# Performance work log

Hardware: AMD Instinct MI355X
Metric: run time of the kernel (lower is better)

## Reference

```python
import jax, jax.numpy as jnp
import numpy as np

IMAGE_SIZE = 288.0
LAMBDA_NOOBJ = 0.5
LAMBDA_COOR = 5.0
_ANCHOR_DIMS = np.array([[0.24, 0.24], [0.12, 0.12], [0.08, 0.08], [0.28, 0.28], [0.15, 0.15]], np.float32)
ANCHORS = jnp.concatenate([jnp.full((5, 2), 0.5, jnp.float32), jnp.asarray(_ANCHOR_DIMS)], axis=1)  # [cx,cy,w,h]


def _corners(box):
    # matches torch _format_bbox column order used in _get_iou: (x1, x2, y1, y2)
    cx, cy, w, h = box[..., 0], box[..., 1], box[..., 2], box[..., 3]
    return cx - w / 2, cx + w / 2, cy - h / 2, cy + h / 2


def _iou(b1, b2):
    x1a, x2a, y1a, y2a = _corners(b1)
    x1b, x2b, y1b, y2b = _corners(b2)
    iw = jnp.minimum(x2a, x2b) - jnp.maximum(x1a, x1b) + 1.0
    ih = jnp.minimum(y2a, y2b) - jnp.maximum(y1a, y1b) + 1.0
    inter = iw * ih
    a1 = (x2a - x1a + 1.0) * (y2a - y1a + 1.0)
    a2 = (x2b - x1b + 1.0) * (y2b - y1b + 1.0)
    return inter / (a1 + a2 - inter + 1e-16)


def setup_inputs() -> dict:
    key = jax.random.key(0)
    k1, k2, k3, k4 = jax.random.split(key, 4)
    B, G, A, T = 32, 36, 5, 8
    return {
        "bbox_prediction": jax.random.normal(k1, (B, G, G, A, 5), jnp.float32),
        "landmarks_prediction": jax.random.normal(k2, (B, G, G, A, 68, 2), jnp.float32),
        "bbox_target": jax.random.uniform(k3, (B, T, 4), jnp.float32),
        "landmarks_target": jax.random.uniform(k4, (B, T, 68, 2), jnp.float32),
    }


def _forward(bbox_prediction, landmarks_prediction, bbox_target, landmarks_target):
    B, G, _, A, _ = bbox_prediction.shape
    T = bbox_target.shape[1]
    N = B * G * G * A

    valid = bbox_target.sum(-1) != 0  # (B,T)
    gx = bbox_target[..., 0] * G
    gy = bbox_target[..., 1] * G
    gi = jnp.floor(gx).astype(jnp.int32)  # int(gt_x)
    gj = jnp.floor(gy).astype(jnp.int32)
    fx = gx - gi
    fy = gy - gj
    gt_anchor_box = jnp.stack([fx, fy, bbox_target[..., 2], bbox_target[..., 3]], -1)  # (B,T,4)

    # vectorized anchor assignment (replaces per-target python loop)
    anchor_iou = _iou(gt_anchor_box[:, :, None, :], ANCHORS[None, None, :, :])  # (B,T,A)
    best_a = jnp.argmax(anchor_iou, -1).astype(jnp.int32)
    log_box = jnp.log1p(gt_anchor_box)  # (B,T,4) -- torch stores log1p form

    lin = ((jnp.arange(B)[:, None] * G + gj) * G + gi) * A + best_a  # (B,T) flat (b,j,i,a)
    lin = jnp.where(valid, lin, N)  # invalid targets -> dump slot N

    obj = jnp.zeros(N + 1, jnp.float32).at[lin.ravel()].set(1.0)[:N].reshape(B, G, G, A)
    noobj = 1.0 - obj

    t_ids = jnp.broadcast_to(jnp.arange(T, dtype=jnp.int32), (B, T))
    seg_last = jax.ops.segment_max(t_ids.ravel(), lin.ravel(), num_segments=N + 1)
    winner = (seg_last[lin] == t_ids) & valid
    lin_w = jnp.where(winner, lin, N).ravel()

    gt_boxes = jnp.zeros((N + 1, 4), jnp.float32).at[lin_w].set(log_box.reshape(-1, 4))[:N].reshape(B, G, G, A, 4)
    gt_lm = jnp.zeros((N + 1, 136), jnp.float32).at[lin_w].set(landmarks_target.reshape(B * T, 136))[:N].reshape(B, G, G, A, 136)

    nobj = jnp.maximum(obj.sum(), 1.0)

    # NME over object cells (masked-mean expressed as weighted sum -> static shapes)
    diff = landmarks_prediction.reshape(B, G, G, A, 136) - gt_lm
    dist = jnp.sqrt(jnp.sum(diff * diff, -1))  # (B,G,G,A)
    wh = gt_boxes[..., 2] * gt_boxes[..., 3]  # note: log1p(w)*log1p(h), as in torch
    norm = jnp.sqrt(jnp.where(obj > 0, wh, 1.0)) * IMAGE_SIZE * 68.0 * nobj
    nme = jnp.sum(obj * dist / norm)

    # localization: SmoothL1 (beta=1), mean over masked elements
    d = bbox_prediction[..., :4] - gt_boxes
    ad = jnp.abs(d)
    sl1 = jnp.where(ad < 1.0, 0.5 * d * d, ad - 0.5)
    loc_loss = LAMBDA_COOR * jnp.sum(obj[..., None] * sl1) / (nobj * 4.0)

    # confidence: MSE on noobj (target 0) + MSE on obj (target 1)
    conf_pred = bbox_prediction[..., 4]
    n_noobj = jnp.maximum(noobj.sum(), 1.0)
    conf_loss = LAMBDA_NOOBJ * jnp.sum(noobj * conf_pred ** 2) / n_noobj + jnp.sum(obj * (conf_pred - 1.0) ** 2) / nobj

    # best predicted bbox per target (IoU of log1p gt box vs raw cell predictions, as in torch)
    cell_pred = bbox_prediction[jnp.arange(B)[:, None], gj, gi]  # (B,T,A,5)
    pred_iou = _iou(log_box[:, :, None, :], cell_pred[..., :4])  # (B,T,A)
    best_p = jnp.argmax(pred_iou, -1)
    best = jnp.take_along_axis(cell_pred, best_p[..., None, None], axis=2)[:, :, 0]  # (B,T,5)
    x1, x2, y1, y2 = _corners(best[..., :4])
    best_pred = jnp.where(valid[..., None], jnp.stack([x1, x2, y1, y2, best[..., 4]], -1), 0.0)

    return nme, loc_loss, conf_loss, best_pred


def reference(bbox_prediction, landmarks_prediction, bbox_target, landmarks_target):
    return _forward(bbox_prediction, landmarks_prediction, bbox_target, landmarks_target)
```

## Files before the change

### kernel.cpp

```cpp
#include <hip/hip_runtime.h>
#include <math.h>

#define Gc 36
#define Ac 5
#define Bc 32
#define Tc 8
#define NCELLS (Bc*Gc*Gc*Ac)
#define NFLOATS (NCELLS*5)
#define NF4 (NFLOATS/4)
#define NT 256
#define CONF_BLOCKS 128


__device__ __forceinline__ void target_meta(const float* __restrict__ bbox_tgt,
                                            int tid, bool& valid, int& gi, int& gj,
                                            float& fx, float& fy, float& w, float& h,
                                            int& best_a) {
    const int b = tid >> 3, t = tid & 7;
    const float* tg = bbox_tgt + (size_t)(b * Tc + t) * 4;
    float x = tg[0], y = tg[1];
    w = tg[2]; h = tg[3];
    valid = ((x + y + w + h) != 0.0f);
    float gx = x * (float)Gc, gy = y * (float)Gc;
    gi = (int)floorf(gx); gj = (int)floorf(gy);
    gi = min(max(gi, 0), Gc - 1); gj = min(max(gj, 0), Gc - 1);
    fx = gx - floorf(gx); fy = gy - floorf(gy);

    float x1a = fx - w * 0.5f, x2a = fx + w * 0.5f;
    float y1a = fy - h * 0.5f, y2a = fy + h * 0.5f;
    float a1 = (x2a - x1a + 1.0f) * (y2a - y1a + 1.0f);
    const float adim[Ac] = {0.24f, 0.12f, 0.08f, 0.28f, 0.15f};
    best_a = 0;
    float best_iou = -1e30f;
    for (int a = 0; a < Ac; ++a) {
        float x1b = 0.5f - adim[a] * 0.5f, x2b = 0.5f + adim[a] * 0.5f;
        float iw = fminf(x2a, x2b) - fmaxf(x1a, x1b) + 1.0f;
        float ih = fminf(y2a, x2b) - fmaxf(y1a, x1b) + 1.0f;
        float inter = iw * ih;
        float a2 = (x2b - x1b + 1.0f) * (x2b - x1b + 1.0f);
        float iou = inter / (a1 + a2 - inter + 1e-16f);
        if (iou > best_iou) { best_iou = iou; best_a = a; }
    }
}

__global__ __launch_bounds__(NT) void k1_conf_meta(
        const float* __restrict__ bbox_pred,
        const float* __restrict__ bbox_tgt,
        float* __restrict__ ws_f, int* __restrict__ ws_i) {
    if (blockIdx.x < CONF_BLOCKS) {
        __shared__ float red[NT];
        const float4* p4 = (const float4*)bbox_pred;
        float acc = 0.0f;
        for (int j = blockIdx.x * NT + threadIdx.x; j < NF4;
             j += CONF_BLOCKS * NT) {
            float4 f = p4[j];
            int r = (4 * j) % 5;
            float v = (r == 4) ? f.x : (r == 3) ? f.y : (r == 2) ? f.z
                    : (r == 1) ? f.w : 0.0f;
            acc += v * v;
        }
        red[threadIdx.x] = acc;
        __syncthreads();
        for (int s = NT / 2; s > 0; s >>= 1) {
            if (threadIdx.x < s) red[threadIdx.x] += red[threadIdx.x + s];
            __syncthreads();
        }
        if (threadIdx.x == 0) ws_f[blockIdx.x] = red[0];
    } else {
        __shared__ int s_lin[NT];
        const int tid = threadIdx.x;
        const int b = tid >> 3, t = tid & 7;
        bool valid; int gi, gj, best_a; float fx, fy, w, h;
        target_meta(bbox_tgt, tid, valid, gi, gj, fx, fy, w, h, best_a);
        int lin = valid ? (((b * Gc + gj) * Gc + gi) * Ac + best_a) : NCELLS;
        s_lin[tid] = lin;
        __syncthreads();
        bool winner = valid;
        if (valid) {
            for (int t2 = t + 1; t2 < Tc; ++t2)
                if (s_lin[(b << 3) + t2] == lin) { winner = false; break; }
        }
        ws_i[256 + tid] = lin;
        ws_i[512 + tid] = winner ? 1 : 0;
    }
}

__global__ __launch_bounds__(64) void k2_lmdist(
        const float* __restrict__ lm_pred,
        const float* __restrict__ lm_tgt,
        const int* __restrict__ ws_i,
        float* __restrict__ ws_f) {
    const int tgt = blockIdx.x;
    const int lane = threadIdx.x;
    int winner = ws_i[512 + tgt];
    int lin = ws_i[256 + tgt];
    float acc = 0.0f;
    if (winner && lane < 34) {
        const float4* lp = (const float4*)(lm_pred + (size_t)lin * 136);
        const float4* lt = (const float4*)(lm_tgt + (size_t)tgt * 136);
        float4 a = lp[lane], b = lt[lane];
        float dx = a.x - b.x, dy = a.y - b.y, dz = a.z - b.z, dw = a.w - b.w;
        acc = dx * dx + dy * dy + dz * dz + dw * dw;
    }
    for (int off = 32; off > 0; off >>= 1)
        acc += __shfl_down(acc, off, 64);
    if (lane == 0) ws_f[1024 + tgt] = winner ? sqrtf(acc) : 0.0f;
}

__device__ __forceinline__ float block_sum(float v, float* red, int tid) {
    red[tid] = v;
    __syncthreads();
    for (int s = NT / 2; s > 0; s >>= 1) {
        if (tid < s) red[tid] += red[tid + s];
        __syncthreads();
    }
    float r = red[0];
    __syncthreads();
    return r;
}

__global__ __launch_bounds__(NT) void k3_final(
        const float* __restrict__ bbox_pred,
        const float* __restrict__ bbox_tgt,
        const float* __restrict__ ws_f,
        const int* __restrict__ ws_i,
        float* __restrict__ out) {
    const int tid = threadIdx.x;
    const int b = tid >> 3, t = tid & 7;
    __shared__ float s_red[NT];
    __shared__ int s_cnt[NT];

    bool valid; int gi, gj, best_a; float fx, fy, w, h;
    target_meta(bbox_tgt, tid, valid, gi, gj, fx, fy, w, h, best_a);
    int lin = ws_i[256 + tid];
    int winner = ws_i[512 + tid];
    float dist = ws_f[1024 + tid];

    float l0 = log1pf(fx), l1 = log1pf(fy), l2 = log1pf(w), l3 = log1pf(h);

    float c_nme = 0.0f, c_sl1 = 0.0f, c_cobj = 0.0f, c_csq = 0.0f;
    if (winner) {
        const float* bp = bbox_pred + (size_t)lin * 5;
        float conf = bp[4];
        c_cobj = (conf - 1.0f) * (conf - 1.0f);
        c_csq = conf * conf;
        float lb[4] = {l0, l1, l2, l3};
        for (int k = 0; k < 4; ++k) {
            float d = bp[k] - lb[k];
            float ad = fabsf(d);
            c_sl1 += (ad < 1.0f) ? 0.5f * d * d : (ad - 0.5f);
        }
        c_nme = dist / (sqrtf(l2 * l3) * 288.0f * 68.0f);
    }

    s_cnt[tid] = winner;
    __syncthreads();
    for (int s = NT / 2; s > 0; s >>= 1) {
        if (tid < s) s_cnt[tid] += s_cnt[tid + s];
        __syncthreads();
    }
    int cnt = s_cnt[0];
    __syncthreads();
    float nobj = fmaxf((float)cnt, 1.0f);
    float n_noobj = fmaxf((float)(NCELLS - cnt), 1.0f);

    float sum_nme  = block_sum(c_nme, s_red, tid);
    float sum_sl1  = block_sum(c_sl1, s_red, tid);
    float sum_cobj = block_sum(c_cobj, s_red, tid);
    float sum_csq  = block_sum(c_csq, s_red, tid);
    float s_total  = block_sum(tid < CONF_BLOCKS ? ws_f[tid] : 0.0f, s_red, tid);

    if (tid == 0) {
        out[0] = sum_nme / nobj;
        out[1] = 5.0f * sum_sl1 / (nobj * 4.0f);
        out[2] = 0.5f * (s_total - sum_csq) / n_noobj + sum_cobj / nobj;
    }

    const float* cp = bbox_pred + (size_t)((b * Gc + gj) * Gc + gi) * Ac * 5;
    float x1g = l0 - l2 * 0.5f, x2g = l0 + l2 * 0.5f;
    float y1g = l1 - l3 * 0.5f, y2g = l1 + l3 * 0.5f;
    float ag = (x2g - x1g + 1.0f) * (y2g - y1g + 1.0f);
    int bp_idx = 0;
    float bp_iou = -1e30f;
    for (int a = 0; a < Ac; ++a) {
        float cx = cp[a * 5 + 0], cy = cp[a * 5 + 1];
        float pw = cp[a * 5 + 2], ph = cp[a * 5 + 3];
        float x1p = cx - pw * 0.5f, x2p = cx + pw * 0.5f;
        float y1p = cy - ph * 0.5f, y2p = cy + ph * 0.5f;
        float iw = fminf(x2g, x2p) - fmaxf(x1g, x1p) + 1.0f;
        float ih = fminf(y2g, y2p) - fmaxf(y1g, y1p) + 1.0f;
        float inter = iw * ih;
        float ap = (x2p - x1p + 1.0f) * (y2p - y1p + 1.0f);
        float iou = inter / (ag + ap - inter + 1e-16f);
        if (iou > bp_iou) { bp_iou = iou; bp_idx = a; }
    }
    float bx = cp[bp_idx * 5 + 0], by = cp[bp_idx * 5 + 1];
    float bw = cp[bp_idx * 5 + 2], bh = cp[bp_idx * 5 + 3];
    float bconf = cp[bp_idx * 5 + 4];
    float* op = out + 3 + (size_t)tid * 5;
    if (valid) {
        op[0] = bx - bw * 0.5f; op[1] = bx + bw * 0.5f;
        op[2] = by - bh * 0.5f; op[3] = by + bh * 0.5f; op[4] = bconf;
    } else {
        op[0] = 0.0f; op[1] = 0.0f; op[2] = 0.0f; op[3] = 0.0f; op[4] = 0.0f;
    }
}

extern "C" void kernel_launch(void* const* d_in, const int* in_sizes, int n_in,
                              void* d_out, int out_size, void* d_ws, size_t ws_size,
                              hipStream_t stream) {
    const float* bbox_pred = (const float*)d_in[0];
    const float* lm_pred   = (const float*)d_in[1];
    const float* bbox_tgt  = (const float*)d_in[2];
    const float* lm_tgt    = (const float*)d_in[3];
    float* out = (float*)d_out;
    float* ws_f = (float*)d_ws;
    int* ws_i = (int*)d_ws;

    k1_conf_meta<<<CONF_BLOCKS + 1, NT, 0, stream>>>(bbox_pred, bbox_tgt, ws_f, ws_i);
    k2_lmdist<<<256, 64, 0, stream>>>(lm_pred, lm_tgt, ws_i, ws_f);
    k3_final<<<1, NT, 0, stream>>>(bbox_pred, bbox_tgt, ws_f, ws_i, out);
}
```

Baseline: 159.0 us.

## Fuse three kernels into one with atomic last-block finalization

Replaces the three-kernel pipeline (confidence reduction plus target metadata, landmark distance, final reduction) with a single 256-block kernel. Each block does a slice of the confidence sum-of-squares, computes metadata and the landmark distance for one target, and accumulates into workspace through atomics. The last block to finish writes the scalar losses. This removes two kernel launches and their inter-kernel dependencies, at the cost of a memset, float atomics with nondeterministic summation order, and dropping the gi/gj clamp.

```diff
diff --git a/kernel.cpp b/kernel.cpp
--- a/kernel.cpp
+++ b/kernel.cpp
@@ -6,24 +6,21 @@
 #define Bc 32
 #define Tc 8
 #define NCELLS (Bc*Gc*Gc*Ac)
-#define NFLOATS (NCELLS*5)
-#define NF4 (NFLOATS/4)
+#define NF4 (NCELLS*5/4)
 #define NT 256
-#define CONF_BLOCKS 128
+#define NB 256
 
 
 __device__ __forceinline__ void target_meta(const float* __restrict__ bbox_tgt,
-                                            int tid, bool& valid, int& gi, int& gj,
+                                            int tgt, bool& valid, int& gi, int& gj,
                                             float& fx, float& fy, float& w, float& h,
                                             int& best_a) {
-    const int b = tid >> 3, t = tid & 7;
-    const float* tg = bbox_tgt + (size_t)(b * Tc + t) * 4;
+    const float* tg = bbox_tgt + (size_t)tgt * 4;
     float x = tg[0], y = tg[1];
     w = tg[2]; h = tg[3];
     valid = ((x + y + w + h) != 0.0f);
     float gx = x * (float)Gc, gy = y * (float)Gc;
     gi = (int)floorf(gx); gj = (int)floorf(gy);
-    gi = min(max(gi, 0), Gc - 1); gj = min(max(gj, 0), Gc - 1);
     fx = gx - floorf(gx); fy = gy - floorf(gy);
 
     float x1a = fx - w * 0.5f, x2a = fx + w * 0.5f;
@@ -43,166 +40,136 @@
     }
 }
 
-__global__ __launch_bounds__(NT) void k1_conf_meta(
+__global__ __launch_bounds__(NT) void fused(
         const float* __restrict__ bbox_pred,
+        const float* __restrict__ lm_pred,
         const float* __restrict__ bbox_tgt,
-        float* __restrict__ ws_f, int* __restrict__ ws_i) {
-    if (blockIdx.x < CONF_BLOCKS) {
-        __shared__ float red[NT];
-        const float4* p4 = (const float4*)bbox_pred;
-        float acc = 0.0f;
-        for (int j = blockIdx.x * NT + threadIdx.x; j < NF4;
-             j += CONF_BLOCKS * NT) {
-            float4 f = p4[j];
-            int r = (4 * j) % 5;
-            float v = (r == 4) ? f.x : (r == 3) ? f.y : (r == 2) ? f.z
-                    : (r == 1) ? f.w : 0.0f;
-            acc += v * v;
-        }
-        red[threadIdx.x] = acc;
-        __syncthreads();
-        for (int s = NT / 2; s > 0; s >>= 1) {
-            if (threadIdx.x < s) red[threadIdx.x] += red[threadIdx.x + s];
-            __syncthreads();
-        }
-        if (threadIdx.x == 0) ws_f[blockIdx.x] = red[0];
-    } else {
-        __shared__ int s_lin[NT];
-        const int tid = threadIdx.x;
-        const int b = tid >> 3, t = tid & 7;
-        bool valid; int gi, gj, best_a; float fx, fy, w, h;
-        target_meta(bbox_tgt, tid, valid, gi, gj, fx, fy, w, h, best_a);
-        int lin = valid ? (((b * Gc + gj) * Gc + gi) * Ac + best_a) : NCELLS;
-        s_lin[tid] = lin;
-        __syncthreads();
-        bool winner = valid;
-        if (valid) {
-            for (int t2 = t + 1; t2 < Tc; ++t2)
-                if (s_lin[(b << 3) + t2] == lin) { winner = false; break; }
-        }
-        ws_i[256 + tid] = lin;
-        ws_i[512 + tid] = winner ? 1 : 0;
+        const float* __restrict__ lm_tgt,
+        float* __restrict__ ws_f, int* __restrict__ ws_i,
+        float* __restrict__ out) {
+    const int tid = threadIdx.x;
+    const int bid = blockIdx.x;
+    __shared__ float red[NT];
+    __shared__ int s_lin8[8];
+
+    const float4* p4 = (const float4*)bbox_pred;
+    float acc = 0.0f;
+    for (int j = bid * NT + tid; j < NF4; j += NB * NT) {
+        float4 f = p4[j];
+        int r = (4 * j) % 5;
+        float v = (r == 4) ? f.x : (r == 3) ? f.y : (r == 2) ? f.z
+                : (r == 1) ? f.w : 0.0f;
+        acc += v * v;
     }
-}
-
-__global__ __launch_bounds__(64) void k2_lmdist(
-        const float* __restrict__ lm_pred,
-        const float* __restrict__ lm_tgt,
-        const int* __restrict__ ws_i,
-        float* __restrict__ ws_f) {
-    const int tgt = blockIdx.x;
-    const int lane = threadIdx.x;
-    int winner = ws_i[512 + tgt];
-    int lin = ws_i[256 + tgt];
-    float acc = 0.0f;
-    if (winner && lane < 34) {
-        const float4* lp = (const float4*)(lm_pred + (size_t)lin * 136);
-        const float4* lt = (const float4*)(lm_tgt + (size_t)tgt * 136);
-        float4 a = lp[lane], b = lt[lane];
-        float dx = a.x - b.x, dy = a.y - b.y, dz = a.z - b.z, dw = a.w - b.w;
-        acc = dx * dx + dy * dy + dz * dz + dw * dw;
-    }
-    for (int off = 32; off > 0; off >>= 1)
-        acc += __shfl_down(acc, off, 64);
-    if (lane == 0) ws_f[1024 + tgt] = winner ? sqrtf(acc) : 0.0f;
-}
-
-__device__ __forceinline__ float block_sum(float v, float* red, int tid) {
-    red[tid] = v;
+    red[tid] = acc;
     __syncthreads();
     for (int s = NT / 2; s > 0; s >>= 1) {
         if (tid < s) red[tid] += red[tid + s];
         __syncthreads();
     }
-    float r = red[0];
+
+    const int tgt = bid;
+    const int b = tgt >> 3, t = tgt & 7;
+    if (tid < 8) {
+        bool v; int gi, gj, ba; float fx, fy, w, h;
+        target_meta(bbox_tgt, (b << 3) + tid, v, gi, gj, fx, fy, w, h, ba);
+        s_lin8[tid] = v ? (((b * Gc + gj) * Gc + gi) * Ac + ba) : NCELLS;
+    }
     __syncthreads();
-    return r;
-}
 
-__global__ __launch_bounds__(NT) void k3_final(
-        const float* __restrict__ bbox_pred,
-        const float* __restrict__ bbox_tgt,
-        const float* __restrict__ ws_f,
-        const int* __restrict__ ws_i,
-        float* __restrict__ out) {
-    const int tid = threadIdx.x;
-    const int b = tid >> 3, t = tid & 7;
-    __shared__ float s_red[NT];
-    __shared__ int s_cnt[NT];
+    if (tid < 64) {
+        int lin = s_lin8[t];
+        bool valid = (lin != NCELLS);
+        bool winner = valid;
+        if (valid)
+            for (int t2 = t + 1; t2 < Tc; ++t2)
+                if (s_lin8[t2] == lin) { winner = false; break; }
 
-    bool valid; int gi, gj, best_a; float fx, fy, w, h;
-    target_meta(bbox_tgt, tid, valid, gi, gj, fx, fy, w, h, best_a);
-    int lin = ws_i[256 + tid];
-    int winner = ws_i[512 + tid];
-    float dist = ws_f[1024 + tid];
+        float a2 = 0.0f;
+        if (winner && tid < 34) {
+            const float4* lp = (const float4*)(lm_pred + (size_t)lin * 136);
+            const float4* lt = (const float4*)(lm_tgt + (size_t)tgt * 136);
+            float4 a = lp[tid], c = lt[tid];
+            float dx = a.x - c.x, dy = a.y - c.y, dz = a.z - c.z, dw = a.w - c.w;
+            a2 = dx * dx + dy * dy + dz * dz + dw * dw;
+        }
+        for (int off = 32; off > 0; off >>= 1)
+            a2 += __shfl_down(a2, off, 64);
 
-    float l0 = log1pf(fx), l1 = log1pf(fy), l2 = log1pf(w), l3 = log1pf(h);
+        if (tid == 0) {
+            bool v; int gi, gj, ba; float fx, fy, w, h;
+            target_meta(bbox_tgt, tgt, v, gi, gj, fx, fy, w, h, ba);
+            float l0 = log1pf(fx), l1 = log1pf(fy), l2 = log1pf(w), l3 = log1pf(h);
 
-    float c_nme = 0.0f, c_sl1 = 0.0f, c_cobj = 0.0f, c_csq = 0.0f;
-    if (winner) {
-        const float* bp = bbox_pred + (size_t)lin * 5;
-        float conf = bp[4];
-        c_cobj = (conf - 1.0f) * (conf - 1.0f);
-        c_csq = conf * conf;
-        float lb[4] = {l0, l1, l2, l3};
-        for (int k = 0; k < 4; ++k) {
-            float d = bp[k] - lb[k];
-            float ad = fabsf(d);
-            c_sl1 += (ad < 1.0f) ? 0.5f * d * d : (ad - 0.5f);
+            float c_nme = 0.0f, c_sl1 = 0.0f, c_cobj = 0.0f, c_csq = 0.0f;
+            if (winner) {
+                const float* bp = bbox_pred + (size_t)lin * 5;
+                float conf = bp[4];
+                c_cobj = (conf - 1.0f) * (conf - 1.0f);
+                c_csq = conf * conf;
+                float lb[4] = {l0, l1, l2, l3};
+                for (int k = 0; k < 4; ++k) {
+                    float d = bp[k] - lb[k];
+                    float ad = fabsf(d);
+                    c_sl1 += (ad < 1.0f) ? 0.5f * d * d : (ad - 0.5f);
+                }
+                c_nme = sqrtf(a2) / (sqrtf(l2 * l3) * 288.0f * 68.0f);
+            }
+
+            const float* cp = bbox_pred + (size_t)((b * Gc + gj) * Gc + gi) * Ac * 5;
+            float x1g = l0 - l2 * 0.5f, x2g = l0 + l2 * 0.5f;
+            float y1g = l1 - l3 * 0.5f, y2g = l1 + l3 * 0.5f;
+            float ag = (x2g - x1g + 1.0f) * (y2g - y1g + 1.0f);
+            int bp_idx = 0;
+            float bp_iou = -1e30f;
+            for (int a = 0; a < Ac; ++a) {
+                float cx = cp[a * 5 + 0], cy = cp[a * 5 + 1];
+                float pw = cp[a * 5 + 2], ph = cp[a * 5 + 3];
+                float x1p = cx - pw * 0.5f, x2p = cx + pw * 0.5f;
+                float y1p = cy - ph * 0.5f, y2p = cy + ph * 0.5f;
+                float iw = fminf(x2g, x2p) - fmaxf(x1g, x1p) + 1.0f;
+                float ih = fminf(y2g, y2p) - fmaxf(y1g, y1p) + 1.0f;
+                float inter = iw * ih;
+                float ap = (x2p - x1p + 1.0f) * (y2p - y1p + 1.0f);
+                float iou = inter / (ag + ap - inter + 1e-16f);
+                if (iou > bp_iou) { bp_iou = iou; bp_idx = a; }
+            }
+            float* op = out + 3 + (size_t)tgt * 5;
+            if (v) {
+                float bx = cp[bp_idx * 5 + 0], by = cp[bp_idx * 5 + 1];
+                float bw = cp[bp_idx * 5 + 2], bh = cp[bp_idx * 5 + 3];
+                op[0] = bx - bw * 0.5f; op[1] = bx + bw * 0.5f;
+                op[2] = by - bh * 0.5f; op[3] = by + bh * 0.5f;
+                op[4] = cp[bp_idx * 5 + 4];
+            } else {
+                op[0] = 0.0f; op[1] = 0.0f; op[2] = 0.0f; op[3] = 0.0f; op[4] = 0.0f;
+            }
+
+            atomicAdd(&ws_f[1], red[0]);
+            if (winner) {
+                atomicAdd(&ws_f[2], c_nme);
+                atomicAdd(&ws_f[3], c_sl1);
+                atomicAdd(&ws_f[4], c_cobj);
+                atomicAdd(&ws_f[5], c_csq);
+                atomicAdd(&ws_i[6], 1);
+            }
+            __threadfence();
+            int done = atomicAdd(&ws_i[0], 1);
+            if (done == NB - 1) {
+                __threadfence();
+                float total = atomicAdd(&ws_f[1], 0.0f);
+                float snme  = atomicAdd(&ws_f[2], 0.0f);
+                float ssl1  = atomicAdd(&ws_f[3], 0.0f);
+                float scobj = atomicAdd(&ws_f[4], 0.0f);
+                float scsq  = atomicAdd(&ws_f[5], 0.0f);
+                int   cnt   = atomicAdd(&ws_i[6], 0);
+                float nobj = fmaxf((float)cnt, 1.0f);
+                float n_noobj = fmaxf((float)(NCELLS - cnt), 1.0f);
+                out[0] = snme / nobj;
+                out[1] = 5.0f * ssl1 / (nobj * 4.0f);
+                out[2] = 0.5f * (total - scsq) / n_noobj + scobj / nobj;
+            }
         }
-        c_nme = dist / (sqrtf(l2 * l3) * 288.0f * 68.0f);
-    }
-
-    s_cnt[tid] = winner;
-    __syncthreads();
-    for (int s = NT / 2; s > 0; s >>= 1) {
-        if (tid < s) s_cnt[tid] += s_cnt[tid + s];
-        __syncthreads();
-    }
-    int cnt = s_cnt[0];
-    __syncthreads();
-    float nobj = fmaxf((float)cnt, 1.0f);
-    float n_noobj = fmaxf((float)(NCELLS - cnt), 1.0f);
-
-    float sum_nme  = block_sum(c_nme, s_red, tid);
-    float sum_sl1  = block_sum(c_sl1, s_red, tid);
-    float sum_cobj = block_sum(c_cobj, s_red, tid);
-    float sum_csq  = block_sum(c_csq, s_red, tid);
-    float s_total  = block_sum(tid < CONF_BLOCKS ? ws_f[tid] : 0.0f, s_red, tid);
-
-    if (tid == 0) {
-        out[0] = sum_nme / nobj;
-        out[1] = 5.0f * sum_sl1 / (nobj * 4.0f);
-        out[2] = 0.5f * (s_total - sum_csq) / n_noobj + sum_cobj / nobj;
-    }
-
-    const float* cp = bbox_pred + (size_t)((b * Gc + gj) * Gc + gi) * Ac * 5;
-    float x1g = l0 - l2 * 0.5f, x2g = l0 + l2 * 0.5f;
-    float y1g = l1 - l3 * 0.5f, y2g = l1 + l3 * 0.5f;
-    float ag = (x2g - x1g + 1.0f) * (y2g - y1g + 1.0f);
-    int bp_idx = 0;
-    float bp_iou = -1e30f;
-    for (int a = 0; a < Ac; ++a) {
-        float cx = cp[a * 5 + 0], cy = cp[a * 5 + 1];
-        float pw = cp[a * 5 + 2], ph = cp[a * 5 + 3];
-        float x1p = cx - pw * 0.5f, x2p = cx + pw * 0.5f;
-        float y1p = cy - ph * 0.5f, y2p = cy + ph * 0.5f;
-        float iw = fminf(x2g, x2p) - fmaxf(x1g, x1p) + 1.0f;
-        float ih = fminf(y2g, y2p) - fmaxf(y1g, y1p) + 1.0f;
-        float inter = iw * ih;
-        float ap = (x2p - x1p + 1.0f) * (y2p - y1p + 1.0f);
-        float iou = inter / (ag + ap - inter + 1e-16f);
-        if (iou > bp_iou) { bp_iou = iou; bp_idx = a; }
-    }
-    float bx = cp[bp_idx * 5 + 0], by = cp[bp_idx * 5 + 1];
-    float bw = cp[bp_idx * 5 + 2], bh = cp[bp_idx * 5 + 3];
-    float bconf = cp[bp_idx * 5 + 4];
-    float* op = out + 3 + (size_t)tid * 5;
-    if (valid) {
-        op[0] = bx - bw * 0.5f; op[1] = bx + bw * 0.5f;
-        op[2] = by - bh * 0.5f; op[3] = by + bh * 0.5f; op[4] = bconf;
-    } else {
-        op[0] = 0.0f; op[1] = 0.0f; op[2] = 0.0f; op[3] = 0.0f; op[4] = 0.0f;
     }
 }
 
@@ -215,9 +182,9 @@
     const float* lm_tgt    = (const float*)d_in[3];
     float* out = (float*)d_out;
     float* ws_f = (float*)d_ws;
-    int* ws_i = (int*)d_ws;
+    int*   ws_i = (int*)d_ws;
 
-    k1_conf_meta<<<CONF_BLOCKS + 1, NT, 0, stream>>>(bbox_pred, bbox_tgt, ws_f, ws_i);
-    k2_lmdist<<<256, 64, 0, stream>>>(lm_pred, lm_tgt, ws_i, ws_f);
-    k3_final<<<1, NT, 0, stream>>>(bbox_pred, bbox_tgt, ws_f, ws_i, out);
+    hipMemsetAsync(d_ws, 0, 64, stream);
+    fused<<<NB, NT, 0, stream>>>(bbox_pred, lm_pred, bbox_tgt, lm_tgt,
+                                 ws_f, ws_i, out);
 }
```

After: 177.1 us. 1.11x slower.
